# Kernel optimization log

Hardware: AMD Instinct MI355X
Metric: run time of the kernel (lower is better)

Reference implementation:

```python
import jax, jax.numpy as jnp
import numpy as np

B, S, D, H = 2, 2048, 2048, 16
HD = D // H            # 128
BLK = 16               # sparsity block size
LOCAL = 4              # num_local_blocks
GLOBAL = 1             # num_global_blocks
ROPE_THETA = 10000.0


def _fixed_layout(num_blocks: int) -> np.ndarray:
    """DeepSpeed FixedSparsityConfig block layout (unidirectional,
    different_layout_per_head=False, num_different_global_patterns=1,
    horizontal_global_attention=False)."""
    layout = np.zeros((num_blocks, num_blocks), dtype=bool)
    # local windows of LOCAL blocks, causal at block granularity inside window
    for w in range(0, num_blocks, LOCAL):
        end = min(w + LOCAL, num_blocks)
        for row in range(w, end):
            layout[row, w:row + 1] = True
    # vertical global columns: last GLOBAL block(s) of each window
    first = LOCAL - GLOBAL  # head % num_different_global_patterns == 0
    stop = num_blocks - (num_blocks % LOCAL)
    for i in range(first, stop, LOCAL):
        layout[i:, i:i + GLOBAL] = True  # unidirectional: rows >= i
    return layout

_LAYOUT = _fixed_layout(S // BLK)  # [num_blocks, num_blocks] bool, static


def _rope(t, cos, sin):
    # t: [B, S, H, HD]; pairs are adjacent (llama complex view)
    tr = t.reshape(B, S, H, HD // 2, 2)
    a, b = tr[..., 0], tr[..., 1]
    c = cos[None, :, None, :]
    s = sin[None, :, None, :]
    out = jnp.stack([a * c - b * s, a * s + b * c], axis=-1)
    return out.reshape(B, S, H, HD)


def setup_inputs() -> dict:
    key = jax.random.key(0)
    kx, kq, kk, kv, ko = jax.random.split(key, 5)
    x = jax.random.normal(kx, (B, S, D), dtype=jnp.float32)
    wscale = 1.0 / np.sqrt(D)
    wq = jax.random.normal(kq, (D, D), dtype=jnp.float32) * wscale
    wk = jax.random.normal(kk, (D, D), dtype=jnp.float32) * wscale
    wv = jax.random.normal(kv, (D, D), dtype=jnp.float32) * wscale
    wo = jax.random.normal(ko, (D, D), dtype=jnp.float32) * wscale
    # rotary tables (freqs_cis split into real/imag parts)
    freqs = 1.0 / (ROPE_THETA ** (np.arange(0, HD, 2, dtype=np.float32) / HD))
    angles = np.arange(S, dtype=np.float32)[:, None] * freqs[None, :]  # [S, HD//2]
    cos = jnp.asarray(np.cos(angles), dtype=jnp.float32)
    sin = jnp.asarray(np.sin(angles), dtype=jnp.float32)
    return {"x": x, "cos": cos, "sin": sin, "wq": wq, "wk": wk, "wv": wv, "wo": wo}


def reference(x, cos, sin, wq, wk, wv, wo):
    xq = (x @ wq).reshape(B, S, H, HD)
    xk = (x @ wk).reshape(B, S, H, HD)
    xv = (x @ wv).reshape(B, S, H, HD)
    xq = _rope(xq, cos, sin)
    xk = _rope(xk, cos, sin)
    # module casts q/k/v to fp16 before the sparse kernel; emulate precision
    xq = xq.astype(jnp.float16).astype(jnp.float32)
    xk = xk.astype(jnp.float16).astype(jnp.float32)
    xv = xv.astype(jnp.float16).astype(jnp.float32)
    q = jnp.transpose(xq, (0, 2, 1, 3))  # [B, H, S, HD]
    k = jnp.transpose(xk, (0, 2, 1, 3))
    v = jnp.transpose(xv, (0, 2, 1, 3))
    scale = 1.0 / np.sqrt(HD)
    scores = jnp.einsum('bhqd,bhkd->bhqk', q, k) * scale
    # block-granularity sparsity mask (DeepSpeed masks only at block level)
    blk = jnp.arange(S) // BLK
    mask = jnp.asarray(_LAYOUT)[blk[:, None], blk[None, :]]  # [S, S] bool
    scores = jnp.where(mask[None, None], scores, -jnp.inf)
    probs = jax.nn.softmax(scores, axis=-1)
    out = jnp.einsum('bhqk,bhkd->bhqd', probs, v)  # [B, H, S, HD]
    out = jnp.transpose(out, (0, 2, 1, 3)).reshape(B, S, D)
    return out @ wo
```

## Files before the change

kernel.cpp:

```cpp
#include <hip/hip_runtime.h>

#define B_ 2
#define S_ 2048
#define D_ 2048
#define H_ 16
#define HD_ 128

typedef _Float16 fp16x2 __attribute__((ext_vector_type(2)));
typedef _Float16 fp16x4 __attribute__((ext_vector_type(4)));
typedef _Float16 fp16x8 __attribute__((ext_vector_type(8)));
typedef float f32x4 __attribute__((ext_vector_type(4)));

__device__ __forceinline__ void gl_lds16(const _Float16* g, _Float16* l) {
  __builtin_amdgcn_global_load_lds((const __attribute__((address_space(1))) void*)g,
                                   (__attribute__((address_space(3))) void*)l, 16, 0, 0);
}

__global__ __launch_bounds__(256) void k_cast(const float* __restrict__ in,
                                              _Float16* __restrict__ out, int n4) {
  int i = blockIdx.x * 256 + threadIdx.x;
  if (i >= n4) return;
  f32x4 v = ((const f32x4*)in)[i];
  fp16x4 h = {(_Float16)v[0], (_Float16)v[1], (_Float16)v[2], (_Float16)v[3]};
  ((fp16x4*)out)[i] = h;
}

__global__ __launch_bounds__(256) void k_trw4(const float* __restrict__ w0,
                                              const float* __restrict__ w1,
                                              const float* __restrict__ w2,
                                              const float* __restrict__ w3,
                                              _Float16* __restrict__ o0,
                                              _Float16* __restrict__ o1,
                                              _Float16* __restrict__ o2,
                                              _Float16* __restrict__ o3) {
  __shared__ float tile[64][65];
  const float* w = (blockIdx.z == 0) ? w0 : (blockIdx.z == 1) ? w1 : (blockIdx.z == 2) ? w2 : w3;
  _Float16* wt = (blockIdx.z == 0) ? o0 : (blockIdx.z == 1) ? o1 : (blockIdx.z == 2) ? o2 : o3;
  int k0 = blockIdx.y * 64, n0 = blockIdx.x * 64;
  int t = threadIdx.x;
  int r = t >> 2, c0 = (t & 3) * 16;
  const float* ip = w + (size_t)(k0 + r) * D_ + n0 + c0;
#pragma unroll
  for (int j = 0; j < 16; j += 4) {
    f32x4 v = *(const f32x4*)(ip + j);
    tile[r][c0 + j] = v[0]; tile[r][c0 + j + 1] = v[1];
    tile[r][c0 + j + 2] = v[2]; tile[r][c0 + j + 3] = v[3];
  }
  __syncthreads();
  _Float16* op = wt + (size_t)(n0 + r) * D_ + k0 + c0;
#pragma unroll
  for (int j = 0; j < 16; j += 8) {
    fp16x8 v;
#pragma unroll
    for (int q = 0; q < 8; ++q) v[q] = (_Float16)tile[c0 + j + q][r];
    *(fp16x8*)(op + j) = v;
  }
}

__global__ __launch_bounds__(512) void k_qkv256(const _Float16* __restrict__ A,
                                                const _Float16* __restrict__ BT,
                                                const float* __restrict__ cosT,
                                                const float* __restrict__ sinT,
                                                _Float16* __restrict__ Qo,
                                                _Float16* __restrict__ Ko,
                                                _Float16* __restrict__ Vo) {
  __shared__ __align__(16) _Float16 smem[65536];
  const int tid = threadIdx.x;
  const int w = tid >> 6, lane = tid & 63;
  const int l15 = lane & 15, lg = lane >> 4;
  const int bid = blockIdx.x;
  const int xcd = bid & 7, j = bid >> 3;
  const int m0 = (j / 3) * 256;
  const int n0 = (xcd * 3 + j % 3) * 256;
  const int wm = (w >> 2) * 128;
  const int wn = (w & 3) * 64;
  const int lr = lane >> 3, lc = lane & 7;
  const int scol = (lc ^ lr) << 3;
  const _Float16* Asrc = A + (size_t)(m0 + w * 8 + lr) * 2048 + scol;
  const _Float16* Bsrc = BT + (size_t)(n0 + w * 8 + lr) * 2048 + scol;
  _Float16* dstA = smem + w * 512;
  _Float16* dstB = smem + 32768 + w * 512;

  auto stageA = [&](int stg, int u, int k0) {
    gl_lds16(Asrc + (size_t)u * 64 * 2048 + k0, dstA + stg * 16384 + u * 4096);
  };
  auto stageB = [&](int stg, int u, int k0) {
    gl_lds16(Bsrc + (size_t)u * 64 * 2048 + k0, dstB + stg * 16384 + u * 4096);
  };

  int aoff[8], boff[4];
#pragma unroll
  for (int mi = 0; mi < 8; ++mi) {
    const int r = wm + mi * 16 + l15;
    aoff[mi] = (r >> 6) * 4096 + (r & 63) * 64;
  }
#pragma unroll
  for (int ni = 0; ni < 4; ++ni) {
    const int r = wn + ni * 16 + l15;
    boff[ni] = (r >> 6) * 4096 + (r & 63) * 64;
  }
  const int swz[2] = {(lg * 8) ^ ((l15 & 7) * 8), (32 + lg * 8) ^ ((l15 & 7) * 8)};

  f32x4 acc[8][4] = {};

#pragma unroll
  for (int u = 0; u < 4; ++u) stageA(0, u, 0);
#pragma unroll
  for (int u = 0; u < 4; ++u) stageB(0, u, 0);

  for (int t = 0; t < 32; ++t) {
    const int cur = t & 1, nxt = cur ^ 1;
    asm volatile("s_waitcnt vmcnt(0)" ::: "memory");
    __builtin_amdgcn_s_barrier();
    const bool pf = (t + 1) < 32;
    const int k1 = (t + 1) * 64;
    const _Float16* sA = smem + cur * 16384;
    const _Float16* sB = smem + 32768 + cur * 16384;
#pragma unroll
    for (int ks = 0; ks < 2; ++ks) {
      fp16x8 af[8], bf[4];
#pragma unroll
      for (int mi = 0; mi < 8; ++mi) af[mi] = *(const fp16x8*)(sA + aoff[mi] + swz[ks]);
#pragma unroll
      for (int ni = 0; ni < 4; ++ni) bf[ni] = *(const fp16x8*)(sB + boff[ni] + swz[ks]);
      if (pf) {
        if (ks == 0) {
#pragma unroll
          for (int u = 0; u < 4; ++u) stageA(nxt, u, k1);
        } else {
#pragma unroll
          for (int u = 0; u < 4; ++u) stageB(nxt, u, k1);
        }
      }
      __builtin_amdgcn_s_setprio(1);
#pragma unroll
      for (int mi = 0; mi < 8; ++mi)
#pragma unroll
        for (int ni = 0; ni < 4; ++ni)
          acc[mi][ni] = __builtin_amdgcn_mfma_f32_16x16x32_f16(af[mi], bf[ni],
                                                               acc[mi][ni], 0, 0, 0);
      __builtin_amdgcn_s_setprio(0);
    }
    __builtin_amdgcn_s_barrier();
  }

  const int region = n0 >> 11;
  if (region < 2) {
    _Float16* Out = (region == 0) ? Qo : Ko;
#pragma unroll
    for (int mi = 0; mi < 8; ++mi)
#pragma unroll
      for (int ni = 0; ni < 4; ++ni) {
        const int col = n0 + wn + 16 * ni + l15;
        const int d = col & 127;
        const int h = (col >> 7) & 15;
        const int dp = d >> 1;
        const bool odd = d & 1;
#pragma unroll
        for (int i = 0; i < 4; ++i) {
          const int row = m0 + wm + 16 * mi + 4 * lg + i;
          const int b = row >> 11, sl = row & 2047;
          const float self = acc[mi][ni][i];
          const float partner = __shfl_xor(self, 1);
          const float c = cosT[sl * 64 + dp], sn = sinT[sl * 64 + dp];
          const float val = odd ? (partner * sn + self * c) : (self * c - partner * sn);
          Out[(((size_t)b * H_ + h) * S_ + sl) * HD_ + d] = (_Float16)val;
        }
      }
  } else {
#pragma unroll
    for (int mi = 0; mi < 8; ++mi)
#pragma unroll
      for (int ni = 0; ni < 4; ++ni) {
        const int col = n0 + wn + 16 * ni + l15;
        const int d = col & 127;
        const int h = (col >> 7) & 15;
        const int row0 = m0 + wm + 16 * mi + 4 * lg;
        const int b = row0 >> 11, sl0 = row0 & 2047;
        const int kb = sl0 >> 4, kin = sl0 & 15;
        fp16x4 v4;
#pragma unroll
        for (int i = 0; i < 4; ++i) v4[i] = (_Float16)acc[mi][ni][i];
        *(fp16x4*)(Vo + ((((size_t)b * H_ + h) * 128 + kb) * 128 + d) * 16 + kin) = v4;
      }
  }
}

__global__ __launch_bounds__(512) void k_gemm_wo(const _Float16* __restrict__ A,
                                                 const _Float16* __restrict__ BT,
                                                 float* __restrict__ Cf) {
  __shared__ __align__(16) _Float16 smem[73728];
  const int tid = threadIdx.x;
  const int w = tid >> 6, lane = tid & 63;
  const int l15 = lane & 15, lg = lane >> 4;
  const int NPX = 2;
  const int bid = blockIdx.x;
  const int xcd = bid & 7, j = bid >> 3;
  const int m0 = (j / NPX) * 256;
  const int n0 = (xcd * NPX + j % NPX) * 128;
  const int wm = (w >> 1) * 64;
  const int wn = (w & 1) * 64;
  const int lr = lane >> 3, lc = lane & 7;
  const int scol = (lc ^ lr) << 3;
  const _Float16* Asrc = A + (size_t)(m0 + w * 8 + lr) * 2048 + scol;
  const _Float16* Bsrc = BT + (size_t)(n0 + w * 8 + lr) * 2048 + scol;
  _Float16* dstA = smem + w * 512;
  _Float16* dstB = smem + 49152 + w * 512;

  auto stageA = [&](int stg, int u, int k0) {
    gl_lds16(Asrc + (size_t)u * 64 * 2048 + k0, dstA + stg * 16384 + u * 4096);
  };
  auto stageB = [&](int stg, int u, int k0) {
    gl_lds16(Bsrc + (size_t)u * 64 * 2048 + k0, dstB + stg * 8192 + u * 4096);
  };

  int aoff[4], boff[4];
#pragma unroll
  for (int mi = 0; mi < 4; ++mi) {
    const int row = wm + mi * 16 + l15;
    aoff[mi] = (row >> 6) * 4096 + (row & 63) * 64;
  }
#pragma unroll
  for (int ni = 0; ni < 4; ++ni) {
    const int row = wn + ni * 16 + l15;
    boff[ni] = (row >> 6) * 4096 + (row & 63) * 64;
  }
  const int swz[2] = {(lg * 8) ^ ((l15 & 7) * 8), (32 + lg * 8) ^ ((l15 & 7) * 8)};

  f32x4 acc[4][4] = {};

#pragma unroll
  for (int u = 0; u < 4; ++u) stageA(0, u, 0);
  stageB(0, 0, 0); stageB(0, 1, 0);
#pragma unroll
  for (int u = 0; u < 4; ++u) stageA(1, u, 64);
  stageB(1, 0, 64); stageB(1, 1, 64);
  asm volatile("s_waitcnt vmcnt(6)" ::: "memory");
  __builtin_amdgcn_s_barrier();

  for (int t = 0; t < 32; ++t) {
    const int cur = t % 3;
    const bool pf = (t + 2) < 32;
    const int spf = (t + 2) % 3, kpf = (t + 2) * 64;
    const _Float16* sA = smem + cur * 16384;
    const _Float16* sB = smem + 49152 + cur * 8192;
#pragma unroll
    for (int ks = 0; ks < 2; ++ks) {
      fp16x8 af[4], bf[4];
#pragma unroll
      for (int mi = 0; mi < 4; ++mi) af[mi] = *(const fp16x8*)(sA + aoff[mi] + swz[ks]);
#pragma unroll
      for (int ni = 0; ni < 4; ++ni) bf[ni] = *(const fp16x8*)(sB + boff[ni] + swz[ks]);
      if (ks == 0) {
        if (pf) { stageA(spf, 0, kpf); stageA(spf, 1, kpf); stageA(spf, 2, kpf); }
      } else {
        if (pf) {
          stageA(spf, 3, kpf); stageB(spf, 0, kpf); stageB(spf, 1, kpf);
          asm volatile("s_waitcnt vmcnt(6)" ::: "memory");
        } else {
          asm volatile("s_waitcnt vmcnt(0)" ::: "memory");
        }
      }
      __builtin_amdgcn_s_barrier();
      __builtin_amdgcn_s_setprio(1);
#pragma unroll
      for (int mi = 0; mi < 4; ++mi)
#pragma unroll
        for (int ni = 0; ni < 4; ++ni)
          acc[mi][ni] = __builtin_amdgcn_mfma_f32_16x16x32_f16(af[mi], bf[ni],
                                                               acc[mi][ni], 0, 0, 0);
      __builtin_amdgcn_s_setprio(0);
      __builtin_amdgcn_s_barrier();
    }
  }

#pragma unroll
  for (int mi = 0; mi < 4; ++mi)
#pragma unroll
    for (int ni = 0; ni < 4; ++ni) {
      const size_t row = m0 + wm + 16 * mi + 4 * lg;
      const size_t col = n0 + wn + 16 * ni + l15;
#pragma unroll
      for (int i = 0; i < 4; ++i)
        Cf[(row + i) * 2048 + col] = acc[mi][ni][i];
    }
}

__global__ __launch_bounds__(256) void k_attn(const _Float16* __restrict__ Q,
                                              const _Float16* __restrict__ K,
                                              const _Float16* __restrict__ Vb,
                                              _Float16* __restrict__ Oa) {
  __shared__ __align__(16) _Float16 sK[2][2][2048];
  __shared__ __align__(16) _Float16 sV[2][2][2048];
  const int p = blockIdx.x;
  const int qgA = 31 - p, qgB = p;
  const int hh = blockIdx.y, b = blockIdx.z;
  const int t = threadIdx.x;
  const int w = t >> 6, lane = t & 63;
  const int l15 = lane & 15, lg = lane >> 4, g4 = lg * 4;
  const size_t bh = (size_t)b * H_ + hh;
  const float scale = 0.08838834764831845f;

  const int qbA = 4 * qgA + w, qbB = 4 * qgB + w;
  const int LA = qgA + 4, LB = qgB + 4;
  const int nchA = (LA + 1) >> 1, nchB = (LB + 1) >> 1;
  const int total = nchA + nchB;

  const _Float16* QpA = Q + (bh * S_ + (size_t)qbA * 16 + l15) * HD_ + lg * 8;
  const _Float16* QpB = Q + (bh * S_ + (size_t)qbB * 16 + l15) * HD_ + lg * 8;
  fp16x8 qfA[4], qfB[4];
#pragma unroll
  for (int dd = 0; dd < 4; ++dd) {
    qfA[dd] = *(const fp16x8*)(QpA + dd * 32);
    qfB[dd] = *(const fp16x8*)(QpB + dd * 32);
  }
  f32x4 o[8] = {};
  float mrun = -3.0e38f, lsum = 0.f;

  const int sr = t >> 4, sc = t & 15;
  const int ksrc_off = sr * 128 + (sc ^ (sr & 7)) * 8;
  const _Float16* Kb_g = K + bh * S_ * HD_;
  const _Float16* Vb_g = Vb + bh * (size_t)(128 * 2048);

  auto kbof = [&](int qg, int idx) { return idx < qg ? 4 * idx + 3 : 3 * qg + idx; };
  auto chunk_kbs = [&](int ci, int& kb0, int& kb1) {
    int qg, cil;
    if (ci < nchA) { qg = qgA; cil = ci; } else { qg = qgB; cil = ci - nchA; }
    const int L = qg + 4;
    const int i0 = 2 * cil, i1 = i0 + 1;
    kb0 = kbof(qg, i0);
    kb1 = (i1 < L) ? kbof(qg, i1) : kb0;
  };
  auto stage = [&](int buf, int ci) {
    int kb0, kb1;
    chunk_kbs(ci, kb0, kb1);
    gl_lds16(Kb_g + (size_t)kb0 * 2048 + ksrc_off, &sK[buf][0][w * 512]);
    gl_lds16(Kb_g + (size_t)kb1 * 2048 + ksrc_off, &sK[buf][1][w * 512]);
    gl_lds16(Vb_g + (size_t)kb0 * 2048 + t * 8, &sV[buf][0][w * 512]);
    gl_lds16(Vb_g + (size_t)kb1 * 2048 + t * 8, &sV[buf][1][w * 512]);
  };
  auto flush = [&](int qb) {
    const float inv = 1.f / lsum;
    f32x4 li;
#pragma unroll
    for (int i = 0; i < 4; ++i) li[i] = __shfl(inv, g4 + i);
    _Float16* Op = Oa + ((size_t)b * S_ + (size_t)qb * 16 + g4) * D_ + (size_t)hh * HD_ + l15;
#pragma unroll
    for (int ni = 0; ni < 8; ++ni)
#pragma unroll
      for (int i = 0; i < 4; ++i)
        Op[(size_t)i * D_ + 16 * ni] = (_Float16)(o[ni][i] * li[i]);
  };

  stage(0, 0);

  for (int ci = 0; ci < total; ++ci) {
    const int cur = ci & 1;
    if (ci == nchA) {
      flush(qbA);
#pragma unroll
      for (int ni = 0; ni < 8; ++ni) o[ni] = f32x4{0.f, 0.f, 0.f, 0.f};
      mrun = -3.0e38f;
      lsum = 0.f;
    }
    if (ci + 1 < total) {
      stage(cur ^ 1, ci + 1);
      asm volatile("s_waitcnt vmcnt(4)" ::: "memory");
    } else {
      asm volatile("s_waitcnt vmcnt(0)" ::: "memory");
    }
    __builtin_amdgcn_s_barrier();

    const bool inA = ci < nchA;
    const int qg = inA ? qgA : qgB;
    const int qb = inA ? qbA : qbB;
    const int cil = inA ? ci : ci - nchA;
    const int L = qg + 4;
    int kb0, kb1;
    chunk_kbs(ci, kb0, kb1);
    const bool v0 = kb0 <= qb;
    const bool v1 = (2 * cil + 1 < L) && (kb1 <= qb);
    f32x4 st[2];
    const float in0 = v0 ? 0.f : -1.0e30f, in1 = v1 ? 0.f : -1.0e30f;
    st[0] = f32x4{in0, in0, in0, in0};
    st[1] = f32x4{in1, in1, in1, in1};

    const char* kl = (const char*)&sK[cur][0][0];
    const int krow = l15 * 256;
#pragma unroll
    for (int dd = 0; dd < 4; ++dd) {
      const int co = ((dd * 4 + lg) ^ (l15 & 7)) * 16;
      fp16x8 k0 = *(const fp16x8*)(kl + krow + co);
      fp16x8 k1 = *(const fp16x8*)(kl + 4096 + krow + co);
      const fp16x8 qf = inA ? qfA[dd] : qfB[dd];
      st[0] = __builtin_amdgcn_mfma_f32_16x16x32_f16(k0, qf, st[0], 0, 0, 0);
      st[1] = __builtin_amdgcn_mfma_f32_16x16x32_f16(k1, qf, st[1], 0, 0, 0);
    }
    float bm = -3.0e38f;
#pragma unroll
    for (int j = 0; j < 2; ++j)
#pragma unroll
      for (int i = 0; i < 4; ++i) {
        st[j][i] *= scale;
        bm = fmaxf(bm, st[j][i]);
      }
    bm = fmaxf(bm, __shfl_xor(bm, 16));
    bm = fmaxf(bm, __shfl_xor(bm, 32));
    const float mnew = fmaxf(mrun, bm);
    const float corr = __expf(mrun - mnew);
    float pr[2][4];
    float ps = 0.f;
#pragma unroll
    for (int j = 0; j < 2; ++j)
#pragma unroll
      for (int i = 0; i < 4; ++i) {
        pr[j][i] = __expf(st[j][i] - mnew);
        ps += pr[j][i];
      }
    ps += __shfl_xor(ps, 16);
    ps += __shfl_xor(ps, 32);
    lsum = lsum * corr + ps;
    mrun = mnew;
    f32x4 c4;
#pragma unroll
    for (int i = 0; i < 4; ++i) c4[i] = __shfl(corr, g4 + i);
#pragma unroll
    for (int ni = 0; ni < 8; ++ni) {
      o[ni][0] *= c4[0]; o[ni][1] *= c4[1]; o[ni][2] *= c4[2]; o[ni][3] *= c4[3];
    }
    fp16x4 ph0 = {(_Float16)pr[0][0], (_Float16)pr[0][1], (_Float16)pr[0][2], (_Float16)pr[0][3]};
    fp16x4 ph1 = {(_Float16)pr[1][0], (_Float16)pr[1][1], (_Float16)pr[1][2], (_Float16)pr[1][3]};
    const char* vl = (const char*)&sV[cur][0][0];
#pragma unroll
    for (int ni = 0; ni < 8; ++ni) {
      const int vo = (16 * ni + l15) * 32 + g4 * 2;
      fp16x4 vv0 = *(const fp16x4*)(vl + vo);
      fp16x4 vv1 = *(const fp16x4*)(vl + 4096 + vo);
      o[ni] = __builtin_amdgcn_mfma_f32_16x16x16f16(ph0, vv0, o[ni], 0, 0, 0);
      o[ni] = __builtin_amdgcn_mfma_f32_16x16x16f16(ph1, vv1, o[ni], 0, 0, 0);
    }
    __builtin_amdgcn_s_barrier();
  }

  flush(qbB);
}

extern "C" void kernel_launch(void* const* d_in, const int* in_sizes, int n_in,
                              void* d_out, int out_size, void* d_ws, size_t ws_size,
                              hipStream_t stream) {
  const float* x = (const float*)d_in[0];
  const float* cosT = (const float*)d_in[1];
  const float* sinT = (const float*)d_in[2];
  const float* wq = (const float*)d_in[3];
  const float* wk = (const float*)d_in[4];
  const float* wv = (const float*)d_in[5];
  const float* wo = (const float*)d_in[6];
  float* out = (float*)d_out;
  char* ws = (char*)d_ws;

  _Float16* x16 = (_Float16*)(ws);
  _Float16* wtq = (_Float16*)(ws + (16ull << 20));
  _Float16* wtk = (_Float16*)(ws + (24ull << 20));
  _Float16* wtv = (_Float16*)(ws + (32ull << 20));
  _Float16* wto = (_Float16*)(ws + (40ull << 20));
  _Float16* Q16 = (_Float16*)(ws + (48ull << 20));
  _Float16* K16 = (_Float16*)(ws + (64ull << 20));
  _Float16* Vb16 = (_Float16*)(ws + (80ull << 20));

  k_cast<<<8192, 256, 0, stream>>>(x, x16, (B_ * S_ * D_) / 4);
  k_trw4<<<dim3(32, 32, 4), 256, 0, stream>>>(wq, wk, wv, wo, wtq, wtk, wtv, wto);

  k_qkv256<<<384, 512, 0, stream>>>(x16, wtq, cosT, sinT, Q16, K16, Vb16);

  _Float16* attn16 = x16;
  k_attn<<<dim3(16, H_, B_), 256, 0, stream>>>(Q16, K16, Vb16, attn16);

  k_gemm_wo<<<256, 512, 0, stream>>>(attn16, wto, out);
}
```

Before: 224.0 us.

## Restructure QKV GEMM main loop into four phases with interleaved barriers

Splits each k-tile iteration of the projection GEMM into four phases over pairs of M-subtiles, loading B fragments once and A fragments per phase, and covering both k-steps inside each phase. Global-to-LDS prefetches are issued in phases 0 and 1, with a vmcnt wait only in the last phase. Each phase adds barriers and a sched_barrier so that waves stay in lockstep and LDS reads overlap with other waves' MFMA bursts. This is meant to hide LDS and global latency better, at the cost of more barriers per iteration.

```diff
diff --git a/kernel.cpp b/kernel.cpp
--- a/kernel.cpp
+++ b/kernel.cpp
@@ -107,41 +107,54 @@
   for (int u = 0; u < 4; ++u) stageA(0, u, 0);
 #pragma unroll
   for (int u = 0; u < 4; ++u) stageB(0, u, 0);
+  asm volatile("s_waitcnt vmcnt(0)" ::: "memory");
+  __builtin_amdgcn_s_barrier();
 
   for (int t = 0; t < 32; ++t) {
     const int cur = t & 1, nxt = cur ^ 1;
-    asm volatile("s_waitcnt vmcnt(0)" ::: "memory");
-    __builtin_amdgcn_s_barrier();
     const bool pf = (t + 1) < 32;
     const int k1 = (t + 1) * 64;
     const _Float16* sA = smem + cur * 16384;
     const _Float16* sB = smem + 32768 + cur * 16384;
-#pragma unroll
-    for (int ks = 0; ks < 2; ++ks) {
-      fp16x8 af[8], bf[4];
-#pragma unroll
-      for (int mi = 0; mi < 8; ++mi) af[mi] = *(const fp16x8*)(sA + aoff[mi] + swz[ks]);
-#pragma unroll
-      for (int ni = 0; ni < 4; ++ni) bf[ni] = *(const fp16x8*)(sB + boff[ni] + swz[ks]);
+    fp16x8 bf[4][2];
+#pragma unroll
+    for (int p = 0; p < 4; ++p) {
+      if (p == 0) {
+#pragma unroll
+        for (int ni = 0; ni < 4; ++ni)
+#pragma unroll
+          for (int ks = 0; ks < 2; ++ks)
+            bf[ni][ks] = *(const fp16x8*)(sB + boff[ni] + swz[ks]);
+      }
+      fp16x8 af[2][2];
+#pragma unroll
+      for (int q = 0; q < 2; ++q)
+#pragma unroll
+        for (int ks = 0; ks < 2; ++ks)
+          af[q][ks] = *(const fp16x8*)(sA + aoff[2 * p + q] + swz[ks]);
       if (pf) {
-        if (ks == 0) {
-#pragma unroll
-          for (int u = 0; u < 4; ++u) stageA(nxt, u, k1);
-        } else {
-#pragma unroll
-          for (int u = 0; u < 4; ++u) stageB(nxt, u, k1);
+        if (p == 0) {
+          stageA(nxt, 0, k1); stageA(nxt, 1, k1); stageA(nxt, 2, k1); stageA(nxt, 3, k1);
+        } else if (p == 1) {
+          stageB(nxt, 0, k1); stageB(nxt, 1, k1); stageB(nxt, 2, k1); stageB(nxt, 3, k1);
         }
       }
+      if (p == 3) asm volatile("s_waitcnt vmcnt(0)" ::: "memory");
+      __builtin_amdgcn_s_barrier();
+      asm volatile("s_waitcnt lgkmcnt(0)" ::: "memory");
+      __builtin_amdgcn_sched_barrier(0);
       __builtin_amdgcn_s_setprio(1);
 #pragma unroll
-      for (int mi = 0; mi < 8; ++mi)
+      for (int q = 0; q < 2; ++q)
 #pragma unroll
         for (int ni = 0; ni < 4; ++ni)
-          acc[mi][ni] = __builtin_amdgcn_mfma_f32_16x16x32_f16(af[mi], bf[ni],
-                                                               acc[mi][ni], 0, 0, 0);
+#pragma unroll
+          for (int ks = 0; ks < 2; ++ks)
+            acc[2 * p + q][ni] = __builtin_amdgcn_mfma_f32_16x16x32_f16(
+                af[q][ks], bf[ni][ks], acc[2 * p + q][ni], 0, 0, 0);
       __builtin_amdgcn_s_setprio(0);
-    }
-    __builtin_amdgcn_s_barrier();
+      __builtin_amdgcn_s_barrier();
+    }
   }
 
   const int region = n0 >> 11;
```

After: 236.5 us. +5.6%, slower.
